# Optimization experiments

Hardware: AMD Instinct MI355X
Metric: run time of the kernel (lower is better)

Reference implementation:

```python
import math
import jax, jax.numpy as jnp
import numpy as np

B, C_IN, H, W = 32, 96, 64, 64
OUT = 128
EXC = int(OUT * 0.8)   # 102 excitatory channels
INH = OUT - EXC        # 26 inhibitory channels
K = 5
PAD = 2                # kernel//2 so all stages keep spatial size


def _sm_kernel(kernel_size=5, sigma_e=1.2, sigma_i=1.4):
    c = kernel_size // 2
    xx, yy = np.meshgrid(np.arange(kernel_size), np.arange(kernel_size), indexing='ij')
    xx = xx.astype(np.float32) - c
    yy = yy.astype(np.float32) - c
    ge = np.exp(-(xx ** 2 + yy ** 2) / (2 * sigma_e ** 2))
    gi = np.exp(-(xx ** 2 + yy ** 2) / (2 * sigma_i ** 2))
    dog = ge / (2 * math.pi * sigma_e ** 2) - gi / (2 * math.pi * sigma_i ** 2)
    dog = dog / dog[c, c]
    return jnp.asarray(dog[None, None], dtype=jnp.float32)  # [1,1,K,K]


def setup_inputs() -> dict:
    key = jax.random.key(0)
    k1, k2, k3, k4 = jax.random.split(key, 4)
    wr = 25.0 / math.sqrt(C_IN * K * K)
    x = jax.random.normal(k1, (B, C_IN, H, W), jnp.float32)
    w_ee = wr * jnp.abs(jax.random.normal(k2, (EXC, C_IN, K, K), jnp.float32))
    w_ei = wr * jnp.abs(jax.random.normal(k3, (INH, EXC, K, K), jnp.float32))
    w_ie = -wr * jnp.abs(jax.random.normal(k4, (EXC, INH, K, K), jnp.float32))
    return {"x": x, "w_ee": w_ee, "w_ei": w_ei, "w_ie": w_ie, "sm_kernel": _sm_kernel()}


def _reflect_pad(x, p):
    if p == 0:
        return x
    return jnp.pad(x, ((0, 0), (0, 0), (p, p), (p, p)), mode='reflect')


def _conv(x, w, pad=0, groups=1):
    return jax.lax.conv_general_dilated(
        x, w, window_strides=(1, 1), padding=[(pad, pad), (pad, pad)],
        dimension_numbers=('NCHW', 'OIHW', 'NCHW'), feature_group_count=groups)


def _forward(x, w_ee, w_ei, w_ie, sm_kernel):
    y_e = _conv(_reflect_pad(x, PAD), w_ee)                 # [B,EXC,H,W], act=Identity
    y_i = jax.nn.relu(_conv(_reflect_pad(y_e, PAD), w_ei))  # [B,INH,H,W]
    y_ie = _conv(_reflect_pad(y_i, PAD), w_ie)              # [B,EXC,H,W]
    y = y_e + y_ie
    # depthwise surround-modulation conv (zero padding, as in F.conv2d)
    w_sm = jnp.tile(sm_kernel, (EXC, 1, 1, 1))              # [EXC,1,K,K]
    y = _conv(y, w_sm, pad=K // 2, groups=EXC)
    return y, y_e, y_i


def reference(x, w_ee, w_ei, w_ie, sm_kernel):
    y, y_e, y_i = _forward(x, w_ee, w_ei, w_ie, sm_kernel)

    # --- hard WTA masks (winner channel per (b,h,w) position) ---
    win_e = jnp.argmax(y_e, axis=1)                                        # [B,H,W]
    mask_e = (jnp.arange(EXC)[None, :, None, None] == win_e[:, None]).astype(y_e.dtype)
    y_wta_e = y_e * mask_e
    win_i = jnp.argmax(jnp.abs(y_i), axis=1)
    mask_i = (jnp.arange(INH)[None, :, None, None] == win_i[:, None]).astype(y_i.dtype)
    y_wta_i = y_i * mask_i

    # --- transpose-conv outer-product trick; with same-size feature maps the
    # conv collapses to a 1x1 full correlation over (b,h,w) -> einsum ---
    yx_ee = jnp.einsum('bchw,behw->ec', x, y_wta_e)[:, :, None, None]      # [EXC,C_IN,1,1]
    yx_ei = jnp.einsum('behw,bihw->ie', y_wta_e, y_wta_i)[:, :, None, None]  # [INH,EXC,1,1]
    yx_ie = jnp.einsum('bihw,behw->ei', y_wta_i, y)[:, :, None, None]      # [EXC,INH,1,1]

    yu_e = jnp.sum(y_wta_e, axis=(0, 2, 3))[:, None, None, None]           # [EXC,1,1,1]
    yu_i = jnp.sum(jnp.abs(y_wta_i), axis=(0, 2, 3))[:, None, None, None]  # [INH,1,1,1]

    upd_ee = yx_ee - yu_e * w_ee   # broadcasts to [EXC,C_IN,K,K]
    upd_ei = yx_ei - yu_i * w_ei
    upd_ie = yx_ie - yu_e * w_ie
    upd_ee = upd_ee / (jnp.abs(upd_ee).max() + 1e-8)
    upd_ei = upd_ei / (jnp.abs(upd_ei).max() + 1e-8)
    upd_ie = upd_ie / (jnp.abs(upd_ie).max() + 1e-8)

    return (y, upd_ee, upd_ei, upd_ie)
```

## Files before the change

### kernel.cpp

```cpp
#include <hip/hip_runtime.h>

#define B_    32
#define CIN_  96
#define EXC_  102
#define INH_  26
#define HH    64
#define WW    64
#define HW_   4096
#define NPOS  (B_*HW_)
#define EEPAD 97
#define NPART 512
#define NEE   (EXC_*CIN_ + EXC_)
#define NIE   (EXC_*INH_)
#define N1U   (EXC_*CIN_*25)
#define N2U   (INH_*EXC_*25)
#define N3U   (EXC_*INH_*25)

typedef short bf8 __attribute__((ext_vector_type(8)));
typedef float f32x4 __attribute__((ext_vector_type(4)));

__device__ __forceinline__ int refl(int i) {
    if (i < 0) i = -i;
    if (i > 63) i = 126 - i;
    return i;
}

__device__ __forceinline__ short f2bf(float f) {
    unsigned u = __float_as_uint(f);
    return (short)((u + 0x7fffu + ((u >> 16) & 1u)) >> 16);
}

__global__ __launch_bounds__(256) void pack_all(
    const float* __restrict__ w_ee, const float* __restrict__ w_ei,
    const float* __restrict__ w_ie, const float* __restrict__ x,
    short* __restrict__ wdst, short* __restrict__ xdst,
    float* __restrict__ zreg)
{
    const int blk = blockIdx.x;
    if (blk < 1800) {
        int gi = blk*256 + threadIdx.x;
        if (gi >= 460800) return;
        const float* src; int N, C, NPAD, CPAD; int idx;
        if (gi < 268800)      { src = w_ee; N = 102; C = 96;  NPAD = 112; CPAD = 96;  idx = gi; }
        else if (gi < 371200) { src = w_ei; N = 26;  C = 102; NPAD = 32;  CPAD = 128; idx = gi - 268800; }
        else                  { src = w_ie; N = 102; C = 26;  NPAD = 112; CPAD = 32;  idx = gi - 371200; }
        int tap = idx / (NPAD*CPAD);
        int rem = idx - tap*(NPAD*CPAD);
        int n = rem / CPAD, c = rem - n*CPAD;
        float f = (n < N && c < C) ? src[((size_t)n*C + c)*25 + tap] : 0.f;
        wdst[gi] = f2bf(f);
    } else if (blk < 3848) {
        int bb = blk - 1800;
        int b = bb >> 6, bx = bb & 63;
        const int pos = bx*64 + (threadIdx.x & 63);
        const int cg0 = threadIdx.x >> 6;
        for (int cg = cg0; cg < 96/8; cg += 4) {
            bf8 v;
#pragma unroll
            for (int j = 0; j < 8; ++j)
                v[j] = f2bf(x[((size_t)b*CIN_ + cg*8 + j)*HW_ + pos]);
            *(bf8*)(&xdst[((size_t)b*HW_ + pos)*96 + cg*8]) = v;
        }
    } else {
        for (int i = threadIdx.x; i < INH_*EXC_ + INH_ + 3; i += 256) zreg[i] = 0.f;
    }
}

template<int C, int CPAD>
__global__ __launch_bounds__(256) void pack_nhwc(
    const float* __restrict__ src, short* __restrict__ dst)
{
    const int b = blockIdx.z;
    const int pos = blockIdx.x*64 + (threadIdx.x & 63);
    const int cg0 = threadIdx.x >> 6;
    for (int cg = cg0; cg < CPAD/8; cg += 4) {
        bf8 v;
#pragma unroll
        for (int j = 0; j < 8; ++j) {
            int c = cg*8 + j;
            float f = (c < C) ? src[((size_t)b*C + c)*HW_ + pos] : 0.f;
            v[j] = f2bf(f);
        }
        *(bf8*)(&dst[((size_t)b*HW_ + pos)*CPAD + cg*8]) = v;
    }
}

template<int CPAD, int NPAD, int NT, int COUT, int NCHUNK,
         bool RELU, bool ADDIN, bool WFLOAT, int OCPAD, bool WTA>
__global__ __launch_bounds__(256, 2) void conv_mfma(
    const short* __restrict__ src, const short* __restrict__ wgt,
    const float* __restrict__ addin, float* __restrict__ out,
    short* __restrict__ nhwc_out, int* __restrict__ win,
    float* __restrict__ val)
{
    __shared__ __align__(16) short sA[400*40];
    const int t  = threadIdx.x;
    const int bx = blockIdx.x;
    const int b  = blockIdx.z;
    const int h0 = (bx >> 2) * 16;
    const int w0 = (bx &  3) * 16;
    const int lane = t & 63;
    const int wv = t >> 6;
    const int nh = lane & 15;
    const int q  = lane >> 4;

    int goff[7], loff[7];
#pragma unroll
    for (int s = 0; s < 7; ++s) {
        int i = t + 256*s;
        if (i < 1600) {
            int rec = i >> 2, seg = i & 3;
            int lh = rec / 20, lw = rec - lh*20;
            int gh = refl(h0 - 2 + lh), gw = refl(w0 - 2 + lw);
            goff[s] = (b*HW_ + gh*WW + gw) * CPAD + seg*8;
            loff[s] = rec*40 + seg*8;
        } else { goff[s] = 0; loff[s] = -1; }
    }

    f32x4 acc[4][NT];
#pragma unroll
    for (int mt = 0; mt < 4; ++mt)
#pragma unroll
        for (int nt = 0; nt < NT; ++nt) {
            f32x4 z = {0.f, 0.f, 0.f, 0.f};
            acc[mt][nt] = z;
        }

    int abase[4];
#pragma unroll
    for (int mt = 0; mt < 4; ++mt)
        abase[mt] = ((wv*4 + mt)*20 + nh)*40 + q*8;

    for (int ck = 0; ck < NCHUNK; ++ck) {
        const int c0 = ck*32;
        __syncthreads();
#pragma unroll
        for (int s = 0; s < 7; ++s)
            if (loff[s] >= 0)
                *(bf8*)(&sA[loff[s]]) = *(const bf8*)(&src[goff[s] + c0]);
        __syncthreads();
        const short* wch = wgt + c0 + nh*CPAD + q*8;
        for (int dh = 0; dh < 5; ++dh) {
#pragma unroll
            for (int dw = 0; dw < 5; ++dw) {
                const int tap = dh*5 + dw;
                bf8 bfr[NT];
#pragma unroll
                for (int nt = 0; nt < NT; ++nt)
                    bfr[nt] = *(const bf8*)(&wch[(size_t)(tap*NPAD + nt*16)*CPAD]);
                bf8 afr[4];
#pragma unroll
                for (int mt = 0; mt < 4; ++mt)
                    afr[mt] = *(const bf8*)(&sA[abase[mt] + (dh*20 + dw)*40]);
#pragma unroll
                for (int mt = 0; mt < 4; ++mt)
#pragma unroll
                    for (int nt = 0; nt < NT; ++nt)
                        acc[mt][nt] = __builtin_amdgcn_mfma_f32_16x16x32_bf16(
                            afr[mt], bfr[nt], acc[mt][nt], 0, 0, 0);
            }
        }
    }

#pragma unroll
    for (int mt = 0; mt < 4; ++mt) {
        const int rowi = h0 + wv*4 + mt;
#pragma unroll
        for (int nt = 0; nt < NT; ++nt) {
            const int chn = nt*16 + nh;
            if (WFLOAT && chn < COUT) {
                size_t obase = ((size_t)(b*COUT + chn))*HW_ + rowi*WW + w0 + q*4;
#pragma unroll
                for (int r = 0; r < 4; ++r) {
                    float v = acc[mt][nt][r];
                    if (RELU) v = fmaxf(v, 0.f);
                    if (ADDIN) v += addin[obase + r];
                    out[obase + r] = v;
                }
            }
            if (OCPAD > 0) {
#pragma unroll
                for (int r = 0; r < 4; ++r) {
                    float v = acc[mt][nt][r];
                    if (RELU) v = fmaxf(v, 0.f);
                    int pos = rowi*WW + w0 + q*4 + r;
                    nhwc_out[((size_t)b*HW_ + pos)*OCPAD + chn] = f2bf(v);
                }
            }
        }
        if (OCPAD > NT*16) {
#pragma unroll
            for (int r = 0; r < 4; ++r) {
                int pos = rowi*WW + w0 + q*4 + r;
                for (int ct = NT*16 + nh; ct < OCPAD; ct += 16)
                    nhwc_out[((size_t)b*HW_ + pos)*OCPAD + ct] = 0;
            }
        }
        if (WTA) {
#pragma unroll
            for (int r = 0; r < 4; ++r) {
                float bv = -3.402823e38f; int bc = 0;
#pragma unroll
                for (int nt = 0; nt < NT; ++nt) {
                    const int chn = nt*16 + nh;
                    float v = acc[mt][nt][r];
                    if (RELU) v = fmaxf(v, 0.f);
                    if (chn < COUT && v > bv) { bv = v; bc = chn; }
                }
#pragma unroll
                for (int off = 1; off < 16; off <<= 1) {
                    float ov = __shfl_xor(bv, off);
                    int   oc = __shfl_xor(bc, off);
                    if (ov > bv || (ov == bv && oc < bc)) { bv = ov; bc = oc; }
                }
                if (nh == 0) {
                    int p = b*HW_ + rowi*WW + w0 + q*4 + r;
                    win[p] = bc; val[p] = bv;
                }
            }
        }
    }
}

__global__ __launch_bounds__(256) void smconv_v2(
    const float* __restrict__ in, const float* __restrict__ sm,
    float* __restrict__ out)
{
    __shared__ __align__(16) float sx[36*36];
    const int tid = threadIdx.x;
    const int tile = blockIdx.x;
    const int e = blockIdx.y;
    const int b = blockIdx.z;
    const int h0 = (tile >> 1) * 32, w0 = (tile & 1) * 32;
    const int r  = tid >> 3;
    const int cg = (tid & 7) * 4;
    const float* inc = in + ((size_t)(b*EXC_ + e))*HW_;
#pragma unroll
    for (int it = 0; it < 6; ++it) {
        int i = tid + it*256;
        if (i < 1296) {
            int lh = i / 36, lw = i - lh*36;
            int gh = h0 - 2 + lh, gw = w0 - 2 + lw;
            float v = 0.f;
            if (gh >= 0 && gh < HH && gw >= 0 && gw < WW) v = inc[gh*WW + gw];
            sx[i] = v;
        }
    }
    __syncthreads();
    float a0 = 0.f, a1 = 0.f, a2 = 0.f, a3 = 0.f;
#pragma unroll
    for (int kh = 0; kh < 5; ++kh) {
        const float4* rowp = (const float4*)(sx + (r + kh)*36 + cg);
        float4 v0 = rowp[0], v1 = rowp[1];
        float xv[8] = {v0.x, v0.y, v0.z, v0.w, v1.x, v1.y, v1.z, v1.w};
#pragma unroll
        for (int kw = 0; kw < 5; ++kw) {
            float wv = sm[kh*5 + kw];
            a0 = fmaf(xv[kw+0], wv, a0);
            a1 = fmaf(xv[kw+1], wv, a1);
            a2 = fmaf(xv[kw+2], wv, a2);
            a3 = fmaf(xv[kw+3], wv, a3);
        }
    }
    size_t oidx = ((size_t)(b*EXC_ + e))*HW_ + (h0 + r)*WW + w0 + cg;
    *(float4*)(out + oidx) = make_float4(a0, a1, a2, a3);
}

__global__ __launch_bounds__(256) void scatter_ee_kernel(
    const float* __restrict__ x, const int* __restrict__ win_e,
    const float* __restrict__ val_e, float* __restrict__ parts)
{
    __shared__ float s_yx[EXC_*EEPAD];
    __shared__ float s_yu[EXC_];
    for (int i = threadIdx.x; i < EXC_*EEPAD; i += 256) s_yx[i] = 0.f;
    if (threadIdx.x < EXC_) s_yu[threadIdx.x] = 0.f;
    __syncthreads();
    int p = blockIdx.x * 256 + threadIdx.x;
    int b = p >> 12, hw = p & 4095;
    int wi = win_e[p]; float v = val_e[p];
    atomicAdd(&s_yu[wi], v);
    const float* xb = x + ((size_t)b*CIN_)*HW_ + hw;
    float* row = s_yx + wi*EEPAD;
    for (int c = 0; c < CIN_; ++c)
        atomicAdd(&row[c], v * xb[(size_t)c*HW_]);
    __syncthreads();
    float* dst = parts + (size_t)blockIdx.x * NEE;
    for (int i = threadIdx.x; i < EXC_*CIN_; i += 256) {
        int e = i / CIN_, c = i - e*CIN_;
        dst[i] = s_yx[e*EEPAD + c];
    }
    if (threadIdx.x < EXC_) dst[EXC_*CIN_ + threadIdx.x] = s_yu[threadIdx.x];
}

__global__ __launch_bounds__(256) void scatter_iei_kernel(
    const float* __restrict__ y, const int* __restrict__ win_e,
    const float* __restrict__ val_e, const int* __restrict__ win_i,
    const float* __restrict__ val_i, float* __restrict__ yx_ei,
    float* __restrict__ yu_i, float* __restrict__ parts)
{
    __shared__ float s_ei[INH_*EXC_ + INH_];
    __shared__ float s_ie[EXC_*INH_];
    for (int i = threadIdx.x; i < INH_*EXC_ + INH_; i += 256) s_ei[i] = 0.f;
    for (int i = threadIdx.x; i < EXC_*INH_; i += 256) s_ie[i] = 0.f;
    __syncthreads();
    int p = blockIdx.x * 256 + threadIdx.x;
    int b = p >> 12, hw = p & 4095;
    int we = win_e[p]; float ve = val_e[p];
    int wi = win_i[p]; float vi = val_i[p];
    atomicAdd(&s_ei[wi*EXC_ + we], ve*vi);
    atomicAdd(&s_ei[INH_*EXC_ + wi], fabsf(vi));
    if (vi != 0.f) {
        const float* yb = y + ((size_t)b*EXC_)*HW_ + hw;
        for (int e = 0; e < EXC_; ++e)
            atomicAdd(&s_ie[e*INH_ + wi], vi * yb[(size_t)e*HW_]);
    }
    __syncthreads();
    for (int i = threadIdx.x; i < INH_*EXC_ + INH_; i += 256) {
        float v = s_ei[i];
        if (v != 0.f) {
            if (i < INH_*EXC_) atomicAdd(&yx_ei[i], v);
            else               atomicAdd(&yu_i[i - INH_*EXC_], v);
        }
    }
    float* dst = parts + (size_t)blockIdx.x * NIE;
    for (int i = threadIdx.x; i < EXC_*INH_; i += 256) dst[i] = s_ie[i];
}

__global__ __launch_bounds__(256) void reduce_all_kernel(
    const float* __restrict__ parts_ee, const float* __restrict__ parts_ie,
    float* __restrict__ yx_ee, float* __restrict__ yx_ie)
{
    __shared__ float s[256];
    int col = blockIdx.x*64 + (threadIdx.x & 63);
    int g = threadIdx.x >> 6;
    const float* P; float* D; int n, i;
    if (col < NEE) { P = parts_ee; D = yx_ee; n = NEE; i = col; }
    else           { P = parts_ie; D = yx_ie; n = NIE; i = col - NEE; }
    float a = 0.f;
    if (col < NEE + NIE) {
        for (int j = g*(NPART/4); j < (g+1)*(NPART/4); ++j)
            a += P[(size_t)j*n + i];
    }
    s[threadIdx.x] = a;
    __syncthreads();
    if (threadIdx.x < 64 && col < NEE + NIE)
        D[i] = s[threadIdx.x] + s[threadIdx.x+64] + s[threadIdx.x+128] + s[threadIdx.x+192];
}

__global__ __launch_bounds__(256) void upd_absmax3(
    const float* __restrict__ yx_ee, const float* __restrict__ yu_e,
    const float* __restrict__ w_ee,
    const float* __restrict__ yx_ei, const float* __restrict__ yu_i,
    const float* __restrict__ w_ei,
    const float* __restrict__ yx_ie, const float* __restrict__ w_ie,
    unsigned int* __restrict__ amax)
{
    float m0 = 0.f, m1 = 0.f, m2 = 0.f;
    for (int idx = blockIdx.x*256 + threadIdx.x; idx < N1U + N2U + N3U;
         idx += gridDim.x*256) {
        if (idx < N1U) {
            int ec = idx / 25; int e = ec / CIN_;
            m0 = fmaxf(m0, fabsf(yx_ee[ec] - yu_e[e]*w_ee[idx]));
        } else if (idx < N1U + N2U) {
            int j = idx - N1U; int ec = j / 25; int e = ec / EXC_;
            m1 = fmaxf(m1, fabsf(yx_ei[ec] - yu_i[e]*w_ei[j]));
        } else {
            int j = idx - N1U - N2U; int ec = j / 25; int e = ec / INH_;
            m2 = fmaxf(m2, fabsf(yx_ie[ec] - yu_e[e]*w_ie[j]));
        }
    }
    __shared__ unsigned int s0, s1, s2;
    if (threadIdx.x == 0) { s0 = 0u; s1 = 0u; s2 = 0u; }
    __syncthreads();
    atomicMax(&s0, __float_as_uint(m0));
    atomicMax(&s1, __float_as_uint(m1));
    atomicMax(&s2, __float_as_uint(m2));
    __syncthreads();
    if (threadIdx.x == 0) {
        atomicMax(&amax[0], s0);
        atomicMax(&amax[1], s1);
        atomicMax(&amax[2], s2);
    }
}

__global__ __launch_bounds__(256) void upd_write3(
    const float* __restrict__ yx_ee, const float* __restrict__ yu_e,
    const float* __restrict__ w_ee,
    const float* __restrict__ yx_ei, const float* __restrict__ yu_i,
    const float* __restrict__ w_ei,
    const float* __restrict__ yx_ie, const float* __restrict__ w_ie,
    const unsigned int* __restrict__ amax,
    float* __restrict__ out_ee, float* __restrict__ out_ei,
    float* __restrict__ out_ie)
{
    int idx = blockIdx.x*256 + threadIdx.x;
    if (idx >= N1U + N2U + N3U) return;
    if (idx < N1U) {
        int ec = idx / 25; int e = ec / CIN_;
        float v = yx_ee[ec] - yu_e[e]*w_ee[idx];
        out_ee[idx] = v / (__uint_as_float(amax[0]) + 1e-8f);
    } else if (idx < N1U + N2U) {
        int j = idx - N1U; int ec = j / 25; int e = ec / EXC_;
        float v = yx_ei[ec] - yu_i[e]*w_ei[j];
        out_ei[j] = v / (__uint_as_float(amax[1]) + 1e-8f);
    } else {
        int j = idx - N1U - N2U; int ec = j / 25; int e = ec / INH_;
        float v = yx_ie[ec] - yu_e[e]*w_ie[j];
        out_ie[j] = v / (__uint_as_float(amax[2]) + 1e-8f);
    }
}

extern "C" void kernel_launch(void* const* d_in, const int* in_sizes, int n_in,
                              void* d_out, int out_size, void* d_ws, size_t ws_size,
                              hipStream_t stream)
{
    const float* x    = (const float*)d_in[0];
    const float* w_ee = (const float*)d_in[1];
    const float* w_ei = (const float*)d_in[2];
    const float* w_ie = (const float*)d_in[3];
    const float* smk  = (const float*)d_in[4];
    float* out = (float*)d_out;

    float* y_e  = (float*)d_ws;
    short* yibf = (short*)(y_e + (size_t)B_*EXC_*HW_);
    short* R    = yibf + (size_t)4194304;
    short* wee  = R + (size_t)16777216;
    short* wei  = wee + 268800;
    short* wie  = wei + 102400;
    int*   win_e = (int*)(wie + 89600);
    float* val_e = (float*)(win_e + NPOS);
    int*   win_i = (int*)(val_e + NPOS);
    float* val_i = (float*)(win_i + NPOS);
    float* yx_ee = val_i + NPOS;
    float* yu_e  = yx_ee + EXC_*CIN_;
    float* yx_ie = yu_e + EXC_;
    float* yx_ei = yx_ie + EXC_*INH_;
    float* yu_i  = yx_ei + INH_*EXC_;
    unsigned int* amax = (unsigned int*)(yu_i + INH_);
    float* parts_ee = y_e;
    float* parts_ie = parts_ee + (size_t)NPART*NEE;

    pack_all<<<3849, 256, 0, stream>>>(w_ee, w_ei, w_ie, x, wee, R, yx_ei);

    conv_mfma<96, 112, 7, EXC_, 3, false, false, true, 0, true>
        <<<dim3(16, 1, B_), 256, 0, stream>>>(R, wee, nullptr, y_e, nullptr,
                                              win_e, val_e);

    pack_nhwc<EXC_, 128><<<dim3(64, 1, B_), 256, 0, stream>>>(y_e, R);

    conv_mfma<128, 32, 2, INH_, 4, true, false, false, 32, true>
        <<<dim3(16, 1, B_), 256, 0, stream>>>(R, wei, nullptr, nullptr, yibf,
                                              win_i, val_i);

    conv_mfma<32, 112, 7, EXC_, 1, false, true, true, 0, false>
        <<<dim3(16, 1, B_), 256, 0, stream>>>(yibf, wie, y_e, y_e, nullptr,
                                              nullptr, nullptr);

    smconv_v2<<<dim3(4, EXC_, B_), 256, 0, stream>>>(y_e, smk, out);

    scatter_ee_kernel<<<NPART, 256, 0, stream>>>(x, win_e, val_e, parts_ee);
    scatter_iei_kernel<<<NPART, 256, 0, stream>>>(out, win_e, val_e, win_i,
                                                  val_i, yx_ei, yu_i, parts_ie);

    reduce_all_kernel<<<(NEE + NIE + 63)/64, 256, 0, stream>>>(
        parts_ee, parts_ie, yx_ee, yx_ie);

    upd_absmax3<<<480, 256, 0, stream>>>(yx_ee, yu_e, w_ee, yx_ei, yu_i, w_ei,
                                         yx_ie, w_ie, amax);
    float* out_ee = out + (size_t)B_*EXC_*HW_;
    float* out_ei = out_ee + N1U;
    float* out_ie = out_ei + N2U;
    upd_write3<<<(N1U + N2U + N3U + 255)/256, 256, 0, stream>>>(
        yx_ee, yu_e, w_ee, yx_ei, yu_i, w_ei, yx_ie, w_ie, amax,
        out_ee, out_ei, out_ie);
}
```

Before: 564.7 us.

## Fuse scatter kernels and emit NHWC bf16 from first conv directly

Merges the two scatter kernels into one so the winner indices and values are read once per position and one launch is saved. When the workspace is large enough, the first conv also writes a bf16 NHWC copy of y_e as an epilogue, so the separate pack_nhwc pass over y_e can be skipped. The cost is more shared memory per block in the fused scatter, which can lower occupancy, plus extra workspace and a second code path chosen by the workspace size.

```diff
diff --git a/kernel.cpp b/kernel.cpp
--- a/kernel.cpp
+++ b/kernel.cpp
@@ -266,55 +266,52 @@
     *(float4*)(out + oidx) = make_float4(a0, a1, a2, a3);
 }
 
-__global__ __launch_bounds__(256) void scatter_ee_kernel(
-    const float* __restrict__ x, const int* __restrict__ win_e,
-    const float* __restrict__ val_e, float* __restrict__ parts)
+__global__ __launch_bounds__(256) void scatter_all_kernel(
+    const float* __restrict__ x, const float* __restrict__ y,
+    const int* __restrict__ win_e, const float* __restrict__ val_e,
+    const int* __restrict__ win_i, const float* __restrict__ val_i,
+    float* __restrict__ yx_ei, float* __restrict__ yu_i,
+    float* __restrict__ parts_ee, float* __restrict__ parts_ie)
 {
     __shared__ float s_yx[EXC_*EEPAD];
     __shared__ float s_yu[EXC_];
+    __shared__ float s_ei[INH_*EXC_ + INH_];
+    __shared__ float s_ie[EXC_*INH_];
     for (int i = threadIdx.x; i < EXC_*EEPAD; i += 256) s_yx[i] = 0.f;
     if (threadIdx.x < EXC_) s_yu[threadIdx.x] = 0.f;
-    __syncthreads();
-    int p = blockIdx.x * 256 + threadIdx.x;
-    int b = p >> 12, hw = p & 4095;
-    int wi = win_e[p]; float v = val_e[p];
-    atomicAdd(&s_yu[wi], v);
-    const float* xb = x + ((size_t)b*CIN_)*HW_ + hw;
-    float* row = s_yx + wi*EEPAD;
-    for (int c = 0; c < CIN_; ++c)
-        atomicAdd(&row[c], v * xb[(size_t)c*HW_]);
-    __syncthreads();
-    float* dst = parts + (size_t)blockIdx.x * NEE;
-    for (int i = threadIdx.x; i < EXC_*CIN_; i += 256) {
-        int e = i / CIN_, c = i - e*CIN_;
-        dst[i] = s_yx[e*EEPAD + c];
-    }
-    if (threadIdx.x < EXC_) dst[EXC_*CIN_ + threadIdx.x] = s_yu[threadIdx.x];
-}
-
-__global__ __launch_bounds__(256) void scatter_iei_kernel(
-    const float* __restrict__ y, const int* __restrict__ win_e,
-    const float* __restrict__ val_e, const int* __restrict__ win_i,
-    const float* __restrict__ val_i, float* __restrict__ yx_ei,
-    float* __restrict__ yu_i, float* __restrict__ parts)
-{
-    __shared__ float s_ei[INH_*EXC_ + INH_];
-    __shared__ float s_ie[EXC_*INH_];
     for (int i = threadIdx.x; i < INH_*EXC_ + INH_; i += 256) s_ei[i] = 0.f;
     for (int i = threadIdx.x; i < EXC_*INH_; i += 256) s_ie[i] = 0.f;
     __syncthreads();
+
     int p = blockIdx.x * 256 + threadIdx.x;
     int b = p >> 12, hw = p & 4095;
     int we = win_e[p]; float ve = val_e[p];
     int wi = win_i[p]; float vi = val_i[p];
+
     atomicAdd(&s_ei[wi*EXC_ + we], ve*vi);
     atomicAdd(&s_ei[INH_*EXC_ + wi], fabsf(vi));
+
+    atomicAdd(&s_yu[we], ve);
+    {
+        const float* xb = x + ((size_t)b*CIN_)*HW_ + hw;
+        float* row = s_yx + we*EEPAD;
+        for (int c = 0; c < CIN_; ++c)
+            atomicAdd(&row[c], ve * xb[(size_t)c*HW_]);
+    }
+
     if (vi != 0.f) {
         const float* yb = y + ((size_t)b*EXC_)*HW_ + hw;
         for (int e = 0; e < EXC_; ++e)
             atomicAdd(&s_ie[e*INH_ + wi], vi * yb[(size_t)e*HW_]);
     }
     __syncthreads();
+
+    float* dee = parts_ee + (size_t)blockIdx.x * NEE;
+    for (int i = threadIdx.x; i < EXC_*CIN_; i += 256) {
+        int e = i / CIN_, c = i - e*CIN_;
+        dee[i] = s_yx[e*EEPAD + c];
+    }
+    if (threadIdx.x < EXC_) dee[EXC_*CIN_ + threadIdx.x] = s_yu[threadIdx.x];
     for (int i = threadIdx.x; i < INH_*EXC_ + INH_; i += 256) {
         float v = s_ei[i];
         if (v != 0.f) {
@@ -322,8 +319,8 @@
             else               atomicAdd(&yu_i[i - INH_*EXC_], v);
         }
     }
-    float* dst = parts + (size_t)blockIdx.x * NIE;
-    for (int i = threadIdx.x; i < EXC_*INH_; i += 256) dst[i] = s_ie[i];
+    float* die = parts_ie + (size_t)blockIdx.x * NIE;
+    for (int i = threadIdx.x; i < EXC_*INH_; i += 256) die[i] = s_ie[i];
 }
 
 __global__ __launch_bounds__(256) void reduce_all_kernel(
@@ -421,10 +418,26 @@
     const float* smk  = (const float*)d_in[4];
     float* out = (float*)d_out;
 
+    const size_t SZ_YE   = (size_t)B_*EXC_*HW_;
+    const size_t SZ_YEBF = (size_t)B_*HW_*128;
+    const size_t SZ_XBF  = (size_t)B_*HW_*96;
+    const size_t SZ_W    = 460800;
+    const size_t need_direct =
+        SZ_YE*4 + SZ_YEBF*2 + SZ_XBF*2 + SZ_W*2 + (size_t)NPOS*16 + 16000*4;
+    const bool direct = (ws_size >= need_direct);
+
     float* y_e  = (float*)d_ws;
-    short* yibf = (short*)(y_e + (size_t)B_*EXC_*HW_);
-    short* R    = yibf + (size_t)4194304;
-    short* wee  = R + (size_t)16777216;
+    short* yebf; short* R;
+    if (direct) {
+        yebf = (short*)(y_e + SZ_YE);
+        R    = yebf + SZ_YEBF;
+    } else {
+        yebf = nullptr;
+        R    = (short*)(y_e + SZ_YE);
+    }
+    short* yibf = direct ? R : R;
+    short* bigR = direct ? R : (R + (size_t)B_*HW_*32);
+    short* wee  = direct ? (R + SZ_XBF) : (bigR + (size_t)16777216);
     short* wei  = wee + 268800;
     short* wie  = wei + 102400;
     int*   win_e = (int*)(wie + 89600);
@@ -440,27 +453,36 @@
     float* parts_ee = y_e;
     float* parts_ie = parts_ee + (size_t)NPART*NEE;
 
-    pack_all<<<3849, 256, 0, stream>>>(w_ee, w_ei, w_ie, x, wee, R, yx_ei);
-
-    conv_mfma<96, 112, 7, EXC_, 3, false, false, true, 0, true>
-        <<<dim3(16, 1, B_), 256, 0, stream>>>(R, wee, nullptr, y_e, nullptr,
-                                              win_e, val_e);
-
-    pack_nhwc<EXC_, 128><<<dim3(64, 1, B_), 256, 0, stream>>>(y_e, R);
-
-    conv_mfma<128, 32, 2, INH_, 4, true, false, false, 32, true>
-        <<<dim3(16, 1, B_), 256, 0, stream>>>(R, wei, nullptr, nullptr, yibf,
-                                              win_i, val_i);
-
-    conv_mfma<32, 112, 7, EXC_, 1, false, true, true, 0, false>
-        <<<dim3(16, 1, B_), 256, 0, stream>>>(yibf, wie, y_e, y_e, nullptr,
-                                              nullptr, nullptr);
+    pack_all<<<3849, 256, 0, stream>>>(w_ee, w_ei, w_ie, x, wee, bigR, yx_ei);
+
+    if (direct) {
+        conv_mfma<96, 112, 7, EXC_, 3, false, false, true, 128, true>
+            <<<dim3(16, 1, B_), 256, 0, stream>>>(bigR, wee, nullptr, y_e, yebf,
+                                                  win_e, val_e);
+        conv_mfma<128, 32, 2, INH_, 4, true, false, false, 32, true>
+            <<<dim3(16, 1, B_), 256, 0, stream>>>(yebf, wei, nullptr, nullptr,
+                                                  yibf, win_i, val_i);
+        conv_mfma<32, 112, 7, EXC_, 1, false, true, true, 0, false>
+            <<<dim3(16, 1, B_), 256, 0, stream>>>(yibf, wie, y_e, y_e, nullptr,
+                                                  nullptr, nullptr);
+    } else {
+        conv_mfma<96, 112, 7, EXC_, 3, false, false, true, 0, true>
+            <<<dim3(16, 1, B_), 256, 0, stream>>>(bigR, wee, nullptr, y_e, nullptr,
+                                                  win_e, val_e);
+        pack_nhwc<EXC_, 128><<<dim3(64, 1, B_), 256, 0, stream>>>(y_e, bigR);
+        conv_mfma<128, 32, 2, INH_, 4, true, false, false, 32, true>
+            <<<dim3(16, 1, B_), 256, 0, stream>>>(bigR, wei, nullptr, nullptr,
+                                                  yibf, win_i, val_i);
+        conv_mfma<32, 112, 7, EXC_, 1, false, true, true, 0, false>
+            <<<dim3(16, 1, B_), 256, 0, stream>>>(yibf, wie, y_e, y_e, nullptr,
+                                                  nullptr, nullptr);
+    }
 
     smconv_v2<<<dim3(4, EXC_, B_), 256, 0, stream>>>(y_e, smk, out);
 
-    scatter_ee_kernel<<<NPART, 256, 0, stream>>>(x, win_e, val_e, parts_ee);
-    scatter_iei_kernel<<<NPART, 256, 0, stream>>>(out, win_e, val_e, win_i,
-                                                  val_i, yx_ei, yu_i, parts_ie);
+    scatter_all_kernel<<<NPART, 256, 0, stream>>>(x, out, win_e, val_e, win_i,
+                                                  val_i, yx_ei, yu_i,
+                                                  parts_ee, parts_ie);
 
     reduce_all_kernel<<<(NEE + NIE + 63)/64, 256, 0, stream>>>(
         parts_ee, parts_ie, yx_ee, yx_ie);
```

After: 551.5 us. -2.3%, faster.
